# Optimization experiments

Hardware: AMD Instinct MI355X
Metric: run time of the kernel (lower is better)

Reference implementation:

```python
import jax, jax.numpy as jnp
import numpy as np

TIME_STEPS = 20
PREDICT_STEPS = 20
REC_MAX_ENC = 2.0 ** (1.0 / TIME_STEPS)
REC_MAX_DEC = 2.0 ** (1.0 / PREDICT_STEPS)
BATCH = 4096
HIDDEN = 1024
IN = 2


def _indrnn_layer(x, W, u, b):
    """One IndRNN layer, seq-first. x: (T,B,I) -> (T,B,H).
    h_t = relu(W x_t + b + u * h_{t-1}), u is elementwise (diagonal) recurrent weight."""
    pre = jnp.einsum('tbi,hi->tbh', x, W) + b  # one big GEMM over all timesteps

    def step(h, p):
        h = jax.nn.relu(p + u * h)
        return h, h

    h0 = jnp.zeros(pre.shape[1:], pre.dtype)
    _, ys = jax.lax.scan(step, h0, pre)
    return ys


def setup_inputs() -> dict:
    key = jax.random.key(0)
    ks = jax.random.split(key, 16)
    f32 = jnp.float32

    def lin_w(k, out_d, in_d):
        return (jax.random.normal(k, (out_d, in_d), f32) / np.sqrt(in_d)).astype(f32)

    def rec_u(k, h, umax):
        return jax.random.uniform(k, (h,), f32, -umax, umax)

    inp = {
        'x': jax.random.normal(ks[0], (TIME_STEPS, BATCH, IN), f32),
        # encoder layers (2)
        'enc_w0': lin_w(ks[1], HIDDEN, IN),
        'enc_u0': rec_u(ks[2], HIDDEN, REC_MAX_ENC),
        'enc_b0': jnp.zeros((HIDDEN,), f32),
        'enc_w1': lin_w(ks[3], HIDDEN, HIDDEN),
        'enc_u1': rec_u(ks[4], HIDDEN, REC_MAX_ENC),
        'enc_b1': jnp.zeros((HIDDEN,), f32),
        # decoder layers (2)
        'dec_w0': lin_w(ks[5], HIDDEN, HIDDEN),
        'dec_u0': rec_u(ks[6], HIDDEN, REC_MAX_DEC),
        'dec_b0': jnp.zeros((HIDDEN,), f32),
        'dec_w1': lin_w(ks[7], HIDDEN, HIDDEN),
        'dec_u1': rec_u(ks[8], HIDDEN, REC_MAX_DEC),
        'dec_b1': jnp.zeros((HIDDEN,), f32),
        # output head: Linear(hidden, 2)
        'out_w': lin_w(ks[9], 2, HIDDEN),
        'out_b': jnp.zeros((2,), f32),
    }
    return inp


def reference(x, enc_w0, enc_u0, enc_b0, enc_w1, enc_u1, enc_b1,
              dec_w0, dec_u0, dec_b0, dec_w1, dec_u1, dec_b1,
              out_w, out_b):
    # encoder: 2-layer IndRNN, seq-first
    y = _indrnn_layer(x, enc_w0, enc_u0, enc_b0)          # (T,B,H)
    y = _indrnn_layer(y, enc_w1, enc_u1, enc_b1)          # (T,B,H)
    # y[:, -1] -> (T,H); .expand(PREDICT_STEPS, -1, H) prepends a dim -> (P,T,H)
    last = y[:, -1]                                        # (T,H)
    temp = jnp.broadcast_to(last, (PREDICT_STEPS,) + last.shape)  # (P,T,H)
    # decoder: 2-layer IndRNN over seq dim P with batch T
    out = _indrnn_layer(temp, dec_w0, dec_u0, dec_b0)
    out = _indrnn_layer(out, dec_w1, dec_u1, dec_b1)       # (P,T,H)
    # out[:, 0] -> (P,H); Linear head -> (P,2)
    predict = out[:, 0] @ out_w.T + out_b
    return predict
```

## Files before the change

kernel.cpp:

```cpp
#include <hip/hip_runtime.h>


#define HID 1024
#define TSTEPS 20

__device__ __forceinline__ float wred64(float v) {
#pragma unroll
    for (int off = 32; off > 0; off >>= 1) v += __shfl_down(v, off, 64);
    return v;
}

__global__ __launch_bounds__(256) void k_enc(
    const float* __restrict__ x, const float* __restrict__ ew0,
    const float* __restrict__ eb0, const float* __restrict__ ew1,
    const float* __restrict__ eb1, const float* __restrict__ ob,
    float* __restrict__ last0, float* __restrict__ out) {
    const int tid = threadIdx.x, wave = tid >> 6, lane = tid & 63;
    __shared__ float v0s[HID];
    __shared__ float red[4];

    if (blockIdx.x == 0 && tid < 2 * TSTEPS) out[tid] = ob[tid & 1];

    const float x0 = x[8190], x1 = x[8191];
#pragma unroll
    for (int i = tid; i < HID / 2; i += 256) {
        float4 w4 = ((const float4*)ew0)[i];
        float2 e2 = ((const float2*)eb0)[i];
        v0s[2 * i + 0] = fmaxf(fmaf(w4.x, x0, fmaf(w4.y, x1, e2.x)), 0.f);
        v0s[2 * i + 1] = fmaxf(fmaf(w4.z, x0, fmaf(w4.w, x1, e2.y)), 0.f);
    }
    __syncthreads();

    const int r = blockIdx.x * 4 + wave;
    const float4* wrow = (const float4*)(ew1 + r * HID);
    const float4* v4 = (const float4*)v0s;
    float s = 0.f;
#pragma unroll
    for (int k = 0; k < 4; ++k) {
        float4 w = wrow[k * 64 + lane], v = v4[k * 64 + lane];
        s = fmaf(w.x, v.x, s); s = fmaf(w.y, v.y, s);
        s = fmaf(w.z, v.z, s); s = fmaf(w.w, v.w, s);
    }
    s = wred64(s);
    if (lane == 0) last0[r] = fmaxf(s + eb1[r], 0.f);
}

__global__ __launch_bounds__(256) void k_dec0(
    const float* __restrict__ last0, const float* __restrict__ dw0,
    const float* __restrict__ du0, const float* __restrict__ db0,
    float* __restrict__ G) {
    const int tid = threadIdx.x, wave = tid >> 6, lane = tid & 63;
    __shared__ float l0[HID];
    ((float4*)l0)[tid] = ((const float4*)last0)[tid];
    __syncthreads();

    const int r = blockIdx.x * 4 + wave;
    const float4* wrow = (const float4*)(dw0 + r * HID);
    const float4* v4 = (const float4*)l0;
    float s = 0.f;
#pragma unroll
    for (int k = 0; k < 4; ++k) {
        float4 w = wrow[k * 64 + lane], v = v4[k * 64 + lane];
        s = fmaf(w.x, v.x, s); s = fmaf(w.y, v.y, s);
        s = fmaf(w.z, v.z, s); s = fmaf(w.w, v.w, s);
    }
    s = wred64(s);
    if (lane == 0) {
        const float p = s + db0[r], uu = du0[r];
        float g = 0.f;
#pragma unroll
        for (int t = 0; t < TSTEPS; ++t) {
            g = fmaxf(fmaf(uu, g, p), 0.f);
            G[t * HID + r] = g;
        }
    }
}

__global__ __launch_bounds__(256) void k_dec1_out(
    const float* __restrict__ G, const float* __restrict__ dw1,
    const float* __restrict__ du1, const float* __restrict__ db1,
    const float* __restrict__ ow, float* __restrict__ out) {
    const int tid = threadIdx.x, wave = tid >> 6, lane = tid & 63;
    const int rA = blockIdx.x * 8 + wave * 2, rB = rA + 1;
    __shared__ float sh[4][TSTEPS][2];

    const float4* wrA = (const float4*)(dw1 + rA * HID);
    const float4* wrB = (const float4*)(dw1 + rB * HID);
    float4 wa[4], wb[4];
#pragma unroll
    for (int k = 0; k < 4; ++k) { wa[k] = wrA[k * 64 + lane]; wb[k] = wrB[k * 64 + lane]; }

    const float uA = du1[rA], bA = db1[rA], o0A = ow[rA], o1A = ow[HID + rA];
    const float uB = du1[rB], bB = db1[rB], o0B = ow[rB], o1B = ow[HID + rB];
    float hA = 0.f, hB = 0.f;

    for (int t = 0; t < TSTEPS; ++t) {
        const float4* gt = (const float4*)(G + t * HID);
        float sA = 0.f, sB = 0.f;
#pragma unroll
        for (int k = 0; k < 4; ++k) {
            float4 g = gt[k * 64 + lane];
            sA = fmaf(wa[k].x, g.x, sA); sA = fmaf(wa[k].y, g.y, sA);
            sA = fmaf(wa[k].z, g.z, sA); sA = fmaf(wa[k].w, g.w, sA);
            sB = fmaf(wb[k].x, g.x, sB); sB = fmaf(wb[k].y, g.y, sB);
            sB = fmaf(wb[k].z, g.z, sB); sB = fmaf(wb[k].w, g.w, sB);
        }
        sA = wred64(sA);
        sB = wred64(sB);
        if (lane == 0) {
            hA = fmaxf(fmaf(uA, hA, sA + bA), 0.f);
            hB = fmaxf(fmaf(uB, hB, sB + bB), 0.f);
            sh[wave][t][0] = fmaf(o0A, hA, o0B * hB);
            sh[wave][t][1] = fmaf(o1A, hA, o1B * hB);
        }
    }
    __syncthreads();
    if (tid < 2 * TSTEPS) {
        const int t = tid >> 1, j = tid & 1;
        float v = sh[0][t][j] + sh[1][t][j] + sh[2][t][j] + sh[3][t][j];
        atomicAdd(&out[t * 2 + j], v);
    }
}

extern "C" void kernel_launch(void* const* d_in, const int* in_sizes, int n_in,
                              void* d_out, int out_size, void* d_ws, size_t ws_size,
                              hipStream_t stream) {
    const float* x      = (const float*)d_in[0];
    const float* enc_w0 = (const float*)d_in[1];
    const float* enc_b0 = (const float*)d_in[3];
    const float* enc_w1 = (const float*)d_in[4];
    const float* enc_b1 = (const float*)d_in[6];
    const float* dec_w0 = (const float*)d_in[7];
    const float* dec_u0 = (const float*)d_in[8];
    const float* dec_b0 = (const float*)d_in[9];
    const float* dec_w1 = (const float*)d_in[10];
    const float* dec_u1 = (const float*)d_in[11];
    const float* dec_b1 = (const float*)d_in[12];
    const float* out_w  = (const float*)d_in[13];
    const float* out_b  = (const float*)d_in[14];
    float* out = (float*)d_out;

    float* ws    = (float*)d_ws;
    float* last0 = ws;
    float* G     = ws + HID;

    k_enc<<<256, 256, 0, stream>>>(x, enc_w0, enc_b0, enc_w1, enc_b1,
                                   out_b, last0, out);
    k_dec0<<<256, 256, 0, stream>>>(last0, dec_w0, dec_u0, dec_b0, G);
    k_dec1_out<<<128, 256, 0, stream>>>(G, dec_w1, dec_u1, dec_b1, out_w, out);
}
```

Before: 109.7 us.

## Parallelize decoder layer-1 over timesteps across waves, serialize recurrence after

The last decoder kernel now has each block own 4 rows, with each wave computing the dot products for a subset of timesteps (5 each) rather than one wave walking all 20 timesteps sequentially. The per-timestep pre-activations go to shared memory, then 4 threads run the cheap elementwise recurrence and the output head. The grid doubles to 256 blocks. This breaks the serial dependency chain of 20 reductions per wave, adding a sync and holding 64 weight registers per thread.

```diff
diff --git a/kernel.cpp b/kernel.cpp
--- a/kernel.cpp
+++ b/kernel.cpp
@@ -17,7 +17,6 @@
     float* __restrict__ last0, float* __restrict__ out) {
     const int tid = threadIdx.x, wave = tid >> 6, lane = tid & 63;
     __shared__ float v0s[HID];
-    __shared__ float red[4];
 
     if (blockIdx.x == 0 && tid < 2 * TSTEPS) out[tid] = ob[tid & 1];
 
@@ -81,44 +80,67 @@
     const float* __restrict__ du1, const float* __restrict__ db1,
     const float* __restrict__ ow, float* __restrict__ out) {
     const int tid = threadIdx.x, wave = tid >> 6, lane = tid & 63;
-    const int rA = blockIdx.x * 8 + wave * 2, rB = rA + 1;
-    __shared__ float sh[4][TSTEPS][2];
+    const int r0 = blockIdx.x * 4;
+    __shared__ float qs[TSTEPS][4];
+    __shared__ float hs[TSTEPS][4];
 
-    const float4* wrA = (const float4*)(dw1 + rA * HID);
-    const float4* wrB = (const float4*)(dw1 + rB * HID);
-    float4 wa[4], wb[4];
+    float4 w[4][4];
 #pragma unroll
-    for (int k = 0; k < 4; ++k) { wa[k] = wrA[k * 64 + lane]; wb[k] = wrB[k * 64 + lane]; }
+    for (int r = 0; r < 4; ++r) {
+        const float4* wr = (const float4*)(dw1 + (r0 + r) * HID);
+#pragma unroll
+        for (int k = 0; k < 4; ++k) w[r][k] = wr[k * 64 + lane];
+    }
 
-    const float uA = du1[rA], bA = db1[rA], o0A = ow[rA], o1A = ow[HID + rA];
-    const float uB = du1[rB], bB = db1[rB], o0B = ow[rB], o1B = ow[HID + rB];
-    float hA = 0.f, hB = 0.f;
-
-    for (int t = 0; t < TSTEPS; ++t) {
+#pragma unroll
+    for (int ti = 0; ti < 5; ++ti) {
+        const int t = wave + ti * 4;
         const float4* gt = (const float4*)(G + t * HID);
-        float sA = 0.f, sB = 0.f;
+        float4 g[4];
 #pragma unroll
-        for (int k = 0; k < 4; ++k) {
-            float4 g = gt[k * 64 + lane];
-            sA = fmaf(wa[k].x, g.x, sA); sA = fmaf(wa[k].y, g.y, sA);
-            sA = fmaf(wa[k].z, g.z, sA); sA = fmaf(wa[k].w, g.w, sA);
-            sB = fmaf(wb[k].x, g.x, sB); sB = fmaf(wb[k].y, g.y, sB);
-            sB = fmaf(wb[k].z, g.z, sB); sB = fmaf(wb[k].w, g.w, sB);
+        for (int k = 0; k < 4; ++k) g[k] = gt[k * 64 + lane];
+        float s[4] = {0.f, 0.f, 0.f, 0.f};
+#pragma unroll
+        for (int r = 0; r < 4; ++r)
+#pragma unroll
+            for (int k = 0; k < 4; ++k) {
+                s[r] = fmaf(w[r][k].x, g[k].x, s[r]);
+                s[r] = fmaf(w[r][k].y, g[k].y, s[r]);
+                s[r] = fmaf(w[r][k].z, g[k].z, s[r]);
+                s[r] = fmaf(w[r][k].w, g[k].w, s[r]);
+            }
+#pragma unroll
+        for (int off = 32; off > 0; off >>= 1) {
+            s[0] += __shfl_down(s[0], off, 64);
+            s[1] += __shfl_down(s[1], off, 64);
+            s[2] += __shfl_down(s[2], off, 64);
+            s[3] += __shfl_down(s[3], off, 64);
         }
-        sA = wred64(sA);
-        sB = wred64(sB);
         if (lane == 0) {
-            hA = fmaxf(fmaf(uA, hA, sA + bA), 0.f);
-            hB = fmaxf(fmaf(uB, hB, sB + bB), 0.f);
-            sh[wave][t][0] = fmaf(o0A, hA, o0B * hB);
-            sh[wave][t][1] = fmaf(o1A, hA, o1B * hB);
+            qs[t][0] = s[0]; qs[t][1] = s[1];
+            qs[t][2] = s[2]; qs[t][3] = s[3];
         }
     }
     __syncthreads();
+
+    if (tid < 4) {
+        const int r = r0 + tid;
+        const float uu = du1[r], bb = db1[r];
+        float h = 0.f;
+#pragma unroll
+        for (int t = 0; t < TSTEPS; ++t) {
+            h = fmaxf(fmaf(uu, h, qs[t][tid] + bb), 0.f);
+            hs[t][tid] = h;
+        }
+    }
+    __syncthreads();
+
     if (tid < 2 * TSTEPS) {
         const int t = tid >> 1, j = tid & 1;
-        float v = sh[0][t][j] + sh[1][t][j] + sh[2][t][j] + sh[3][t][j];
-        atomicAdd(&out[t * 2 + j], v);
+        const float* owj = ow + j * HID + r0;
+        float p = owj[0] * hs[t][0] + owj[1] * hs[t][1]
+                + owj[2] * hs[t][2] + owj[3] * hs[t][3];
+        atomicAdd(&out[t * 2 + j], p);
     }
 }
 
@@ -147,5 +169,5 @@
     k_enc<<<256, 256, 0, stream>>>(x, enc_w0, enc_b0, enc_w1, enc_b1,
                                    out_b, last0, out);
     k_dec0<<<256, 256, 0, stream>>>(last0, dec_w0, dec_u0, dec_b0, G);
-    k_dec1_out<<<128, 256, 0, stream>>>(G, dec_w1, dec_u1, dec_b1, out_w, out);
+    k_dec1_out<<<256, 256, 0, stream>>>(G, dec_w1, dec_u1, dec_b1, out_w, out);
 }
```

New measurement: 102.3 us. 1.07x faster.
